# Kernel tuning notes

Hardware: AMD Instinct MI355X
Metric: run time of the kernel (lower is better)

## Reference

```python
import jax, jax.numpy as jnp
import numpy as np

N = 4_000_000

def setup_inputs() -> dict:
    key = jax.random.key(0)
    k1, k2, k3, k4 = jax.random.split(key, 4)
    return {
        "rot_kf": jax.random.normal(k1, (N, 3, 3), dtype=jnp.float32),
        "pose_kf": jax.random.normal(k2, (N, 3), dtype=jnp.float32),
        "rot_gt": jax.random.normal(k3, (N, 3, 3), dtype=jnp.float32),
        "pose_gt": jax.random.normal(k4, (N, 3), dtype=jnp.float32),
    }


def reference(rot_kf, pose_kf, rot_gt, pose_gt):
    # Per frame i: M_kf_inv @ M_gt where M_kf_inv = [R_kf^T, -R_kf^T p_kf; 0 1]
    # => relative rotation R_rel = R_kf^T @ R_gt
    #    relative translation t_rel = R_kf^T @ (p_gt - p_kf)
    # ||relative_se3 - I4||_F^2 = ||R_rel - I3||_F^2 + ||t_rel||^2
    # (bottom row [0,0,0,1] matches identity exactly)
    R_rel = jnp.einsum('nji,njk->nik', rot_kf, rot_gt)          # [N,3,3]
    t_rel = jnp.einsum('nji,nj->ni', rot_kf, pose_gt - pose_kf)  # [N,3]
    eye3 = jnp.eye(3, dtype=R_rel.dtype)
    s_error = jnp.sum((R_rel - eye3) ** 2, axis=(1, 2)) + jnp.sum(t_rel ** 2, axis=1)  # [N]
    return jnp.sqrt(jnp.mean(s_error)) + 1e-8
```

## Files before the change

kernel.cpp:

```cpp
#include <hip/hip_runtime.h>
#include <math.h>

#define BLOCK 256
#define FPT   4
#define FPC   1024
#define F4_PER_STAGE 2304
#define MAXBLOCKS 2048

#define GLOAD_LDS16(gp, lp)                                                     \
  __builtin_amdgcn_global_load_lds(                                             \
      (const __attribute__((address_space(1))) void*)(gp),                      \
      (__attribute__((address_space(3))) void*)(lp), 16, 0, 0)

__global__ __launch_bounds__(BLOCK, 2) void rmse_partial_kernel(
    const float* __restrict__ rot_kf, const float* __restrict__ pose_kf,
    const float* __restrict__ rot_gt, const float* __restrict__ pose_gt,
    float* __restrict__ partial, int N)
{
    __shared__ float lds[2][FPC * 9];
    __shared__ float redbuf[BLOCK / 64];

    const int tid = threadIdx.x;
    const long long totalRotF = (long long)N * 9;
    const long long f4max = (totalRotF >= 4) ? (totalRotF - 4) / 4 : 0;
    const int nChunks = (int)(((long long)N + FPC - 1) / FPC);
    const int stride = gridDim.x;

    float sum = 0.0f;

    auto issue = [&](const float* __restrict__ src, float* ldsBuf, int cc) {
        const long long base4 = (long long)cc * F4_PER_STAGE;
        #pragma unroll
        for (int j = 0; j < 9; ++j) {
            long long f4 = base4 + j * BLOCK + tid;
            if (f4 > f4max) f4 = f4max;
            GLOAD_LDS16(reinterpret_cast<const float4*>(src) + f4,
                        ldsBuf + (size_t)(j * BLOCK + tid) * 4);
        }
    };

    int c = blockIdx.x;
    if (c < nChunks) {
        issue(rot_kf, lds[0], c);
        issue(rot_gt, lds[1], c);
    }

    while (c < nChunks) {
        const int cn = c + stride;
        const bool hasNext = (cn < nChunks);

        asm volatile("s_waitcnt vmcnt(9)" ::: "memory");
        __builtin_amdgcn_sched_barrier(0);
        __builtin_amdgcn_s_barrier();

        float a[FPT][9];
        #pragma unroll
        for (int s = 0; s < FPT; ++s) {
            #pragma unroll
            for (int j = 0; j < 9; ++j) a[s][j] = lds[0][(s * BLOCK + tid) * 9 + j];
        }
        asm volatile("s_waitcnt lgkmcnt(0)" ::: "memory");
        __builtin_amdgcn_sched_barrier(0);
        __builtin_amdgcn_s_barrier();
        if (hasNext) issue(rot_kf, lds[0], cn);

        if (hasNext) { asm volatile("s_waitcnt vmcnt(9)" ::: "memory"); }
        else         { asm volatile("s_waitcnt vmcnt(0)" ::: "memory"); }
        __builtin_amdgcn_sched_barrier(0);
        __builtin_amdgcn_s_barrier();

        #pragma unroll
        for (int s = 0; s < FPT; ++s) {
            const int frame = c * FPC + s * BLOCK + tid;
            if (frame < N) {
                float b[9];
                #pragma unroll
                for (int j = 0; j < 9; ++j) b[j] = lds[1][(s * BLOCK + tid) * 9 + j];

                const long long p = (long long)frame * 3;
                const float d0 = pose_gt[p + 0] - pose_kf[p + 0];
                const float d1 = pose_gt[p + 1] - pose_kf[p + 1];
                const float d2 = pose_gt[p + 2] - pose_kf[p + 2];

                float se = 0.0f;
                #pragma unroll
                for (int i = 0; i < 3; ++i) {
                    #pragma unroll
                    for (int k = 0; k < 3; ++k) {
                        float r = a[s][i] * b[k] + a[s][3 + i] * b[3 + k] + a[s][6 + i] * b[6 + k];
                        r -= (i == k) ? 1.0f : 0.0f;
                        se += r * r;
                    }
                    const float t = a[s][i] * d0 + a[s][3 + i] * d1 + a[s][6 + i] * d2;
                    se += t * t;
                }
                sum += se;
            }
        }
        asm volatile("s_waitcnt lgkmcnt(0)" ::: "memory");
        __builtin_amdgcn_sched_barrier(0);
        __builtin_amdgcn_s_barrier();
        if (hasNext) issue(rot_gt, lds[1], cn);

        c = cn;
    }

    const int lane = tid & 63;
    const int wave = tid >> 6;
    #pragma unroll
    for (int off = 32; off > 0; off >>= 1) sum += __shfl_down(sum, off);
    if (lane == 0) redbuf[wave] = sum;
    __syncthreads();
    if (tid == 0) {
        float s = 0.0f;
        #pragma unroll
        for (int w = 0; w < BLOCK / 64; ++w) s += redbuf[w];
        partial[blockIdx.x] = s;
    }
}

__global__ __launch_bounds__(BLOCK) void rmse_finalize_kernel(
    const float* __restrict__ partial, int nPartial, float* __restrict__ out, int N)
{
    __shared__ float redbuf[BLOCK / 64];
    float sum = 0.0f;
    for (int i = threadIdx.x; i < nPartial; i += BLOCK) sum += partial[i];
    #pragma unroll
    for (int off = 32; off > 0; off >>= 1) sum += __shfl_down(sum, off);
    const int lane = threadIdx.x & 63;
    const int wave = threadIdx.x >> 6;
    if (lane == 0) redbuf[wave] = sum;
    __syncthreads();
    if (threadIdx.x == 0) {
        float s = 0.0f;
        #pragma unroll
        for (int w = 0; w < BLOCK / 64; ++w) s += redbuf[w];
        out[0] = sqrtf(s / (float)N) + 1e-8f;
    }
}

extern "C" void kernel_launch(void* const* d_in, const int* in_sizes, int n_in,
                              void* d_out, int out_size, void* d_ws, size_t ws_size,
                              hipStream_t stream) {
    const float* rot_kf  = (const float*)d_in[0];
    const float* pose_kf = (const float*)d_in[1];
    const float* rot_gt  = (const float*)d_in[2];
    const float* pose_gt = (const float*)d_in[3];
    float* out = (float*)d_out;
    float* partial = (float*)d_ws;

    const int N = in_sizes[1] / 3;
    const int nChunks = (int)(((long long)N + FPC - 1) / FPC);

    int grid = (nChunks + 1) / 2;
    if (grid > MAXBLOCKS) grid = MAXBLOCKS;
    const int wsCap = (int)(ws_size / sizeof(float));
    if (grid > wsCap) grid = wsCap;
    if (grid < 1) grid = 1;

    rmse_partial_kernel<<<grid, BLOCK, 0, stream>>>(rot_kf, pose_kf, rot_gt, pose_gt, partial, N);
    rmse_finalize_kernel<<<1, BLOCK, 0, stream>>>(partial, grid, out, N);
}
```

Measured before the change: 74.90 us.

## Switch to single-wave blocks with barrier-free double-buffered LDS prefetch of all inputs

Result: slower. 79.10 us (+5.6%).

```diff
diff --git a/kernel.cpp b/kernel.cpp
--- a/kernel.cpp
+++ b/kernel.cpp
@@ -1,130 +1,147 @@
 #include <hip/hip_runtime.h>
 #include <math.h>
 
-#define BLOCK 256
-#define FPT   4
-#define FPC   1024
-#define F4_PER_STAGE 2304
-#define MAXBLOCKS 2048
+#define WBLOCK 64
+#define FPCW   256
+#define F4_ROT 576
+#define F4_POSE 192
+#define MAXGRID 768
 
 #define GLOAD_LDS16(gp, lp)                                                     \
   __builtin_amdgcn_global_load_lds(                                             \
       (const __attribute__((address_space(1))) void*)(gp),                      \
       (__attribute__((address_space(3))) void*)(lp), 16, 0, 0)
 
-__global__ __launch_bounds__(BLOCK, 2) void rmse_partial_kernel(
+__global__ __launch_bounds__(WBLOCK) void rmse_partial_kernel(
     const float* __restrict__ rot_kf, const float* __restrict__ pose_kf,
     const float* __restrict__ rot_gt, const float* __restrict__ pose_gt,
     float* __restrict__ partial, int N)
 {
-    __shared__ float lds[2][FPC * 9];
-    __shared__ float redbuf[BLOCK / 64];
+    __shared__ float4 ldsA[2][F4_ROT];
+    __shared__ float4 ldsB[2][F4_ROT];
+    __shared__ float4 ldsPK[2][F4_POSE];
+    __shared__ float4 ldsPG[2][F4_POSE];
 
-    const int tid = threadIdx.x;
-    const long long totalRotF = (long long)N * 9;
-    const long long f4max = (totalRotF >= 4) ? (totalRotF - 4) / 4 : 0;
-    const int nChunks = (int)(((long long)N + FPC - 1) / FPC);
+    const int lane = threadIdx.x;
+    const long long rotF4max  = ((long long)N * 9 >= 4) ? ((long long)N * 9 - 4) / 4 : 0;
+    const long long poseF4max = ((long long)N * 3 >= 4) ? ((long long)N * 3 - 4) / 4 : 0;
+    const int nChunks = (int)(((long long)N + FPCW - 1) / FPCW);
     const int stride = gridDim.x;
 
-    float sum = 0.0f;
-
-    auto issue = [&](const float* __restrict__ src, float* ldsBuf, int cc) {
-        const long long base4 = (long long)cc * F4_PER_STAGE;
+    auto issueAll = [&](int cc, int par) {
+        const long long rb = (long long)cc * F4_ROT;
         #pragma unroll
         for (int j = 0; j < 9; ++j) {
-            long long f4 = base4 + j * BLOCK + tid;
-            if (f4 > f4max) f4 = f4max;
-            GLOAD_LDS16(reinterpret_cast<const float4*>(src) + f4,
-                        ldsBuf + (size_t)(j * BLOCK + tid) * 4);
+            long long f4 = rb + j * WBLOCK + lane;
+            if (f4 > rotF4max) f4 = rotF4max;
+            GLOAD_LDS16(reinterpret_cast<const float4*>(rot_kf) + f4,
+                        (void*)&ldsA[par][j * WBLOCK + lane]);
+        }
+        #pragma unroll
+        for (int j = 0; j < 9; ++j) {
+            long long f4 = rb + j * WBLOCK + lane;
+            if (f4 > rotF4max) f4 = rotF4max;
+            GLOAD_LDS16(reinterpret_cast<const float4*>(rot_gt) + f4,
+                        (void*)&ldsB[par][j * WBLOCK + lane]);
+        }
+        const long long pb = (long long)cc * F4_POSE;
+        #pragma unroll
+        for (int j = 0; j < 3; ++j) {
+            long long f4 = pb + j * WBLOCK + lane;
+            if (f4 > poseF4max) f4 = poseF4max;
+            GLOAD_LDS16(reinterpret_cast<const float4*>(pose_kf) + f4,
+                        (void*)&ldsPK[par][j * WBLOCK + lane]);
+        }
+        #pragma unroll
+        for (int j = 0; j < 3; ++j) {
+            long long f4 = pb + j * WBLOCK + lane;
+            if (f4 > poseF4max) f4 = poseF4max;
+            GLOAD_LDS16(reinterpret_cast<const float4*>(pose_gt) + f4,
+                        (void*)&ldsPG[par][j * WBLOCK + lane]);
         }
     };
 
+    float sum = 0.0f;
     int c = blockIdx.x;
-    if (c < nChunks) {
-        issue(rot_kf, lds[0], c);
-        issue(rot_gt, lds[1], c);
-    }
+    int par = 0;
+
+    if (c < nChunks) issueAll(c, 0);
 
     while (c < nChunks) {
         const int cn = c + stride;
         const bool hasNext = (cn < nChunks);
 
-        asm volatile("s_waitcnt vmcnt(9)" ::: "memory");
+        if (hasNext) issueAll(cn, par ^ 1);
+
+        if (hasNext) { asm volatile("s_waitcnt vmcnt(24)" ::: "memory"); }
+        else         { asm volatile("s_waitcnt vmcnt(0)"  ::: "memory"); }
         __builtin_amdgcn_sched_barrier(0);
-        __builtin_amdgcn_s_barrier();
 
-        float a[FPT][9];
+        float4 ta[9], tb[9], tk[3], tg[3];
         #pragma unroll
-        for (int s = 0; s < FPT; ++s) {
-            #pragma unroll
-            for (int j = 0; j < 9; ++j) a[s][j] = lds[0][(s * BLOCK + tid) * 9 + j];
+        for (int j = 0; j < 9; ++j) ta[j] = ldsA[par][lane * 9 + j];
+        #pragma unroll
+        for (int j = 0; j < 9; ++j) tb[j] = ldsB[par][lane * 9 + j];
+        #pragma unroll
+        for (int j = 0; j < 3; ++j) tk[j] = ldsPK[par][lane * 3 + j];
+        #pragma unroll
+        for (int j = 0; j < 3; ++j) tg[j] = ldsPG[par][lane * 3 + j];
+
+        float af[36], bf[36], kf[12], gf[12];
+        #pragma unroll
+        for (int j = 0; j < 9; ++j) {
+            af[4*j] = ta[j].x; af[4*j+1] = ta[j].y; af[4*j+2] = ta[j].z; af[4*j+3] = ta[j].w;
+            bf[4*j] = tb[j].x; bf[4*j+1] = tb[j].y; bf[4*j+2] = tb[j].z; bf[4*j+3] = tb[j].w;
         }
-        asm volatile("s_waitcnt lgkmcnt(0)" ::: "memory");
-        __builtin_amdgcn_sched_barrier(0);
-        __builtin_amdgcn_s_barrier();
-        if (hasNext) issue(rot_kf, lds[0], cn);
+        #pragma unroll
+        for (int j = 0; j < 3; ++j) {
+            kf[4*j] = tk[j].x; kf[4*j+1] = tk[j].y; kf[4*j+2] = tk[j].z; kf[4*j+3] = tk[j].w;
+            gf[4*j] = tg[j].x; gf[4*j+1] = tg[j].y; gf[4*j+2] = tg[j].z; gf[4*j+3] = tg[j].w;
+        }
 
-        if (hasNext) { asm volatile("s_waitcnt vmcnt(9)" ::: "memory"); }
-        else         { asm volatile("s_waitcnt vmcnt(0)" ::: "memory"); }
-        __builtin_amdgcn_sched_barrier(0);
-        __builtin_amdgcn_s_barrier();
-
+        const int fbase = c * FPCW + lane * 4;
         #pragma unroll
-        for (int s = 0; s < FPT; ++s) {
-            const int frame = c * FPC + s * BLOCK + tid;
-            if (frame < N) {
-                float b[9];
-                #pragma unroll
-                for (int j = 0; j < 9; ++j) b[j] = lds[1][(s * BLOCK + tid) * 9 + j];
-
-                const long long p = (long long)frame * 3;
-                const float d0 = pose_gt[p + 0] - pose_kf[p + 0];
-                const float d1 = pose_gt[p + 1] - pose_kf[p + 1];
-                const float d2 = pose_gt[p + 2] - pose_kf[p + 2];
-
+        for (int s = 0; s < 4; ++s) {
+            if (fbase + s < N) {
+                const float* a = &af[s * 9];
+                const float* b = &bf[s * 9];
+                const float d0 = gf[s*3+0] - kf[s*3+0];
+                const float d1 = gf[s*3+1] - kf[s*3+1];
+                const float d2 = gf[s*3+2] - kf[s*3+2];
                 float se = 0.0f;
                 #pragma unroll
                 for (int i = 0; i < 3; ++i) {
                     #pragma unroll
                     for (int k = 0; k < 3; ++k) {
-                        float r = a[s][i] * b[k] + a[s][3 + i] * b[3 + k] + a[s][6 + i] * b[6 + k];
+                        float r = a[i] * b[k] + a[3+i] * b[3+k] + a[6+i] * b[6+k];
                         r -= (i == k) ? 1.0f : 0.0f;
                         se += r * r;
                     }
-                    const float t = a[s][i] * d0 + a[s][3 + i] * d1 + a[s][6 + i] * d2;
+                    const float t = a[i] * d0 + a[3+i] * d1 + a[6+i] * d2;
                     se += t * t;
                 }
                 sum += se;
             }
         }
+
         asm volatile("s_waitcnt lgkmcnt(0)" ::: "memory");
         __builtin_amdgcn_sched_barrier(0);
-        __builtin_amdgcn_s_barrier();
-        if (hasNext) issue(rot_gt, lds[1], cn);
 
         c = cn;
+        par ^= 1;
     }
 
-    const int lane = tid & 63;
-    const int wave = tid >> 6;
     #pragma unroll
     for (int off = 32; off > 0; off >>= 1) sum += __shfl_down(sum, off);
-    if (lane == 0) redbuf[wave] = sum;
-    __syncthreads();
-    if (tid == 0) {
-        float s = 0.0f;
-        #pragma unroll
-        for (int w = 0; w < BLOCK / 64; ++w) s += redbuf[w];
-        partial[blockIdx.x] = s;
-    }
+    if (lane == 0) partial[blockIdx.x] = sum;
 }
 
-__global__ __launch_bounds__(BLOCK) void rmse_finalize_kernel(
+__global__ __launch_bounds__(256) void rmse_finalize_kernel(
     const float* __restrict__ partial, int nPartial, float* __restrict__ out, int N)
 {
-    __shared__ float redbuf[BLOCK / 64];
+    __shared__ float redbuf[4];
     float sum = 0.0f;
-    for (int i = threadIdx.x; i < nPartial; i += BLOCK) sum += partial[i];
+    for (int i = threadIdx.x; i < nPartial; i += 256) sum += partial[i];
     #pragma unroll
     for (int off = 32; off > 0; off >>= 1) sum += __shfl_down(sum, off);
     const int lane = threadIdx.x & 63;
@@ -132,9 +149,7 @@
     if (lane == 0) redbuf[wave] = sum;
     __syncthreads();
     if (threadIdx.x == 0) {
-        float s = 0.0f;
-        #pragma unroll
-        for (int w = 0; w < BLOCK / 64; ++w) s += redbuf[w];
+        float s = redbuf[0] + redbuf[1] + redbuf[2] + redbuf[3];
         out[0] = sqrtf(s / (float)N) + 1e-8f;
     }
 }
@@ -150,14 +165,14 @@
     float* partial = (float*)d_ws;
 
     const int N = in_sizes[1] / 3;
-    const int nChunks = (int)(((long long)N + FPC - 1) / FPC);
+    const int nChunks = (int)(((long long)N + FPCW - 1) / FPCW);
 
-    int grid = (nChunks + 1) / 2;
-    if (grid > MAXBLOCKS) grid = MAXBLOCKS;
+    int grid = MAXGRID;
+    if (grid > nChunks) grid = nChunks;
     const int wsCap = (int)(ws_size / sizeof(float));
     if (grid > wsCap) grid = wsCap;
     if (grid < 1) grid = 1;
 
-    rmse_partial_kernel<<<grid, BLOCK, 0, stream>>>(rot_kf, pose_kf, rot_gt, pose_gt, partial, N);
-    rmse_finalize_kernel<<<1, BLOCK, 0, stream>>>(partial, grid, out, N);
+    rmse_partial_kernel<<<grid, WBLOCK, 0, stream>>>(rot_kf, pose_kf, rot_gt, pose_gt, partial, N);
+    rmse_finalize_kernel<<<1, 256, 0, stream>>>(partial, grid, out, N);
 }
```
